# Optimization experiments

Measured on AMD Instinct MI355X. Metric: run time of the kernel, lower is better.

The kernel has to match this reference:

```python
import jax, jax.numpy as jnp
import numpy as np

B, S, D = 4, 1024, 2048
NH, NKV, HD = 16, 8, 128
N_EXP, TOP_K, RANK, ALPHA = 4, 2, 16, 32
LORA_SCALE = ALPHA / RANK
EPS = 1e-6
NEG_INF = -1e9


def setup_inputs() -> dict:
    key = jax.random.key(0)
    ks = jax.random.split(key, 12)
    inv_freq = 1.0 / (10000.0 ** (jnp.arange(0, HD, 2, dtype=jnp.float32) / HD))
    pos = jnp.arange(S, dtype=jnp.float32)
    freqs = pos[:, None] * inv_freq[None, :]            # [S, HD/2]
    emb = jnp.concatenate([freqs, freqs], axis=-1)      # [S, HD]
    cos = jnp.broadcast_to(jnp.cos(emb)[None], (B, S, HD))
    sin = jnp.broadcast_to(jnp.sin(emb)[None], (B, S, HD))
    s = 0.02
    return {
        "hidden_states": jax.random.normal(ks[0], (B, S, D), jnp.float32),
        "cos": cos,
        "sin": sin,
        "Wq": jax.random.normal(ks[1], (NH * HD, D), jnp.float32) * s,
        "Wk": jax.random.normal(ks[2], (NKV * HD, D), jnp.float32) * s,
        "Wv": jax.random.normal(ks[3], (NKV * HD, D), jnp.float32) * s,
        "Wo": jax.random.normal(ks[4], (D, NH * HD), jnp.float32) * s,
        "q_norm_w": jnp.ones((HD,), jnp.float32),
        "k_norm_w": jnp.ones((HD,), jnp.float32),
        "gate_w": jax.random.normal(ks[5], (N_EXP, D), jnp.float32) * s,
        "loraA": jax.random.normal(ks[6], (N_EXP, RANK, NH * HD), jnp.float32) * s,
        "loraB": jax.random.normal(ks[7], (N_EXP, D, RANK), jnp.float32) * s,
    }


def _rms_norm(x, w):
    # per-head-dim RMSNorm (Qwen3 style), computed in fp32
    var = jnp.mean(jnp.square(x.astype(jnp.float32)), axis=-1, keepdims=True)
    return (x.astype(jnp.float32) * jax.lax.rsqrt(var + EPS)).astype(x.dtype) * w


def _rotate_half(x):
    x1, x2 = jnp.split(x, 2, axis=-1)
    return jnp.concatenate([-x2, x1], axis=-1)


def reference(hidden_states, cos, sin, Wq, Wk, Wv, Wo, q_norm_w, k_norm_w, gate_w, loraA, loraB):
    b, s, d = hidden_states.shape
    scaling = HD ** -0.5

    # ---- router (top-k of softmax over 4 experts) ----
    flat = hidden_states.reshape(-1, d)                       # [T, D]
    router_logits = flat @ gate_w.T                           # [T, E]
    probs = jax.nn.softmax(router_logits.astype(jnp.float32), axis=-1)
    top_w, top_idx = jax.lax.top_k(probs, TOP_K)              # [T, K]
    top_w = top_w.astype(hidden_states.dtype)
    # dense per-expert weight: [T, E]
    expert_w = jnp.sum(jax.nn.one_hot(top_idx, N_EXP, dtype=top_w.dtype) * top_w[..., None], axis=1)

    # ---- QKV projections + per-head RMSNorm ----
    q = (hidden_states @ Wq.T).reshape(b, s, NH, HD)
    k = (hidden_states @ Wk.T).reshape(b, s, NKV, HD)
    v = (hidden_states @ Wv.T).reshape(b, s, NKV, HD)
    q = _rms_norm(q, q_norm_w).transpose(0, 2, 1, 3)          # [B, NH, S, HD]
    k = _rms_norm(k, k_norm_w).transpose(0, 2, 1, 3)          # [B, NKV, S, HD]
    v = v.transpose(0, 2, 1, 3)

    # ---- RoPE ----
    c, sn = cos[:, None], sin[:, None]                        # [B, 1, S, HD]
    q = q * c + _rotate_half(q) * sn
    k = k * c + _rotate_half(k) * sn

    # ---- GQA repeat + eager attention ----
    n_rep = NH // NKV
    k = jnp.repeat(k, n_rep, axis=1)
    v = jnp.repeat(v, n_rep, axis=1)
    attn = jnp.einsum('bhqd,bhkd->bhqk', q, k) * scaling
    causal = jnp.tril(jnp.ones((s, s), bool))
    attn = jnp.where(causal[None, None], attn, NEG_INF)
    attn_w = jax.nn.softmax(attn.astype(jnp.float32), axis=-1).astype(q.dtype)
    attn_out = jnp.einsum('bhqk,bhkd->bqhd', attn_w, v).reshape(b, s, NH * HD)

    # ---- base output projection + LoRA expert mixture ----
    base = attn_out @ Wo.T                                    # [B, S, D]
    x = attn_out.reshape(-1, NH * HD)                         # [T, NH*HD]
    h = jnp.einsum('td,erd->ter', x, loraA)                   # [T, E, R]
    delta = jnp.einsum('ter,edr->ted', h, loraB) * LORA_SCALE # [T, E, D]
    expert_out = jnp.einsum('te,ted->td', expert_w, delta).reshape(b, s, d)

    return base + expert_out
```

## Files before the change

kernel.cpp:

```cpp
#include <hip/hip_runtime.h>
#include <hip/hip_bf16.h>

#define S_LEN   1024
#define BATCH   4
#define DMODEL  2048
#define NHEADS  16
#define NKVH    8
#define HEADD   128
#define NTOK    4096
#define QKV_CH  4096

typedef __bf16 bf16x8 __attribute__((ext_vector_type(8)));
typedef float  f32x4  __attribute__((ext_vector_type(4)));

__device__ __forceinline__ float bf2f(unsigned short u) {
    return __uint_as_float(((unsigned)u) << 16);
}
__device__ __forceinline__ ushort f2bu(float f) {
    union { __hip_bfloat16 h; ushort u; } c;
    c.h = __float2bfloat16(f);
    return c.u;
}
__device__ __forceinline__ void gl_lds16(const ushort* g, ushort* l) {
    __builtin_amdgcn_global_load_lds(
        (const __attribute__((address_space(1))) void*)g,
        (__attribute__((address_space(3))) void*)l,
        16, 0, 0);
}

__global__ __launch_bounds__(256) void wcast_kernel(const float* __restrict__ Wq,
                                                    const float* __restrict__ Wk,
                                                    const float* __restrict__ Wv,
                                                    const float* __restrict__ Wo,
                                                    const float* __restrict__ lA,
                                                    __hip_bfloat16* __restrict__ wqkv,
                                                    __hip_bfloat16* __restrict__ wo,
                                                    __hip_bfloat16* __restrict__ acat) {
    int i = blockIdx.x * 256 + threadIdx.x;
    const float* src; __hip_bfloat16* dst; int off;
    if (i < 1048576)      { src = Wq; dst = wqkv;           off = i; }
    else if (i < 1572864) { src = Wk; dst = wqkv + 4194304; off = i - 1048576; }
    else if (i < 2097152) { src = Wv; dst = wqkv + 6291456; off = i - 1572864; }
    else if (i < 3145728) { src = Wo; dst = wo;             off = i - 2097152; }
    else if (i < 3178496) { src = lA; dst = acat;           off = i - 3145728; }
    else return;
    float4 v = ((const float4*)src)[off];
    union { ushort4 u; __hip_bfloat16 h[4]; } r;
    r.h[0] = __float2bfloat16(v.x);
    r.h[1] = __float2bfloat16(v.y);
    r.h[2] = __float2bfloat16(v.z);
    r.h[3] = __float2bfloat16(v.w);
    ((ushort4*)dst)[off] = r.u;
}

__global__ __launch_bounds__(256) void btrans_kernel(const float* __restrict__ lB,
                                                     const float* __restrict__ cosb,
                                                     const float* __restrict__ sinb,
                                                     ushort* __restrict__ Bt,
                                                     float4* __restrict__ cs4) {
    if (blockIdx.x < 512) {
        int idx = blockIdx.x * 256 + threadIdx.x;
        int d = idx >> 6, er = idx & 63;
        int e = er >> 4, r = er & 15;
        Bt[idx] = f2bu(lB[((size_t)e * DMODEL + d) * 16 + r]);
    } else {
        int idx = (blockIdx.x - 512) * 256 + threadIdx.x;
        int s = idx >> 6, d0 = idx & 63;
        const float* cp = cosb + (size_t)s * HEADD;
        const float* sp = sinb + (size_t)s * HEADD;
        cs4[idx] = make_float4(cp[d0], cp[d0 + 64], sp[d0], sp[d0 + 64]);
    }
}

__global__ __launch_bounds__(256) void gatecast_kernel(const float* __restrict__ X,
                                                       const float* __restrict__ GW,
                                                       __hip_bfloat16* __restrict__ Xb,
                                                       float* __restrict__ EW) {
    __shared__ float red[4][257];
    const int t = blockIdx.x, tid = threadIdx.x;
    const float* x = X + (size_t)t * DMODEL;
    __hip_bfloat16* xb = Xb + (size_t)t * DMODEL;
    float p0 = 0.f, p1 = 0.f, p2 = 0.f, p3 = 0.f;
#pragma unroll
    for (int c = 0; c < 2; c++) {
        int i4 = tid + c * 256;
        float4 v = ((const float4*)x)[i4];
        union { ushort4 u; __hip_bfloat16 h[4]; } r;
        r.h[0] = __float2bfloat16(v.x);
        r.h[1] = __float2bfloat16(v.y);
        r.h[2] = __float2bfloat16(v.z);
        r.h[3] = __float2bfloat16(v.w);
        ((ushort4*)xb)[i4] = r.u;
        int d = i4 * 4;
        const float* g0 = GW + d;
        p0 += v.x * g0[0] + v.y * g0[1] + v.z * g0[2] + v.w * g0[3];
        const float* g1 = GW + DMODEL + d;
        p1 += v.x * g1[0] + v.y * g1[1] + v.z * g1[2] + v.w * g1[3];
        const float* g2 = GW + 2 * DMODEL + d;
        p2 += v.x * g2[0] + v.y * g2[1] + v.z * g2[2] + v.w * g2[3];
        const float* g3 = GW + 3 * DMODEL + d;
        p3 += v.x * g3[0] + v.y * g3[1] + v.z * g3[2] + v.w * g3[3];
    }
    red[0][tid] = p0; red[1][tid] = p1; red[2][tid] = p2; red[3][tid] = p3;
    __syncthreads();
    for (int s = 128; s > 0; s >>= 1) {
        if (tid < s) {
            red[0][tid] += red[0][tid + s];
            red[1][tid] += red[1][tid + s];
            red[2][tid] += red[2][tid + s];
            red[3][tid] += red[3][tid + s];
        }
        __syncthreads();
    }
    if (tid == 0) {
        float l[4] = { red[0][0], red[1][0], red[2][0], red[3][0] };
        float mx = fmaxf(fmaxf(l[0], l[1]), fmaxf(l[2], l[3]));
        float pe[4], sum = 0.f;
        for (int e = 0; e < 4; e++) { pe[e] = __expf(l[e] - mx); sum += pe[e]; }
        float inv = 1.0f / sum;
        for (int e = 0; e < 4; e++) pe[e] *= inv;
        int i1 = 0;
        for (int e = 1; e < 4; e++) if (pe[e] > pe[i1]) i1 = e;
        int i2 = -1;
        for (int e = 0; e < 4; e++) if (e != i1 && (i2 < 0 || pe[e] > pe[i2])) i2 = e;
        float o[4] = {0.f, 0.f, 0.f, 0.f};
        o[i1] = pe[i1]; o[i2] = pe[i2];
        float* ew = EW + (size_t)t * 4;
        ew[0] = o[0]; ew[1] = o[1]; ew[2] = o[2]; ew[3] = o[3];
    }
}

#define LDSA0 0
#define LDSB0 16384
#define LDSA1 32768
#define LDSB1 49152

#define FENCE_BAR() do { asm volatile("" ::: "memory"); __builtin_amdgcn_s_barrier(); } while (0)

__device__ __forceinline__ void stage_half(const ushort* src, ushort* dst, size_t ld) {
    gl_lds16(src, dst);
    gl_lds16(src + (size_t)64 * ld, dst + 4096);
}

#define PHASE_MFMA_PRE()  do { \
    asm volatile("" ::: "memory"); \
    __builtin_amdgcn_s_barrier(); \
    asm volatile("s_waitcnt lgkmcnt(0)" ::: "memory"); \
    __builtin_amdgcn_sched_barrier(0); \
    __builtin_amdgcn_s_setprio(1); } while (0)

#define PHASE_MFMA_POST() do { \
    __builtin_amdgcn_s_setprio(0); } while (0)

__device__ __forceinline__ void ktile(const ushort* As, const ushort* Bs,
                                      f32x4 (&acc)[8][4],
                                      int aBase, int bBase, int cs0, int cs1,
                                      const ushort* s1s, ushort* s1d, bool s12en,
                                      const ushort* s2s, ushort* s2d,
                                      const ushort* s3s, ushort* s3d, bool s34en,
                                      const ushort* s4s, ushort* s4d,
                                      int K, bool lastVm)
{
    bf16x8 a0[4][2], a1[4][2], b0[2][2], b1[2][2];

#pragma unroll
    for (int ii = 0; ii < 4; ii++) {
        a0[ii][0] = *(const bf16x8*)(As + aBase + ii * 2048 + cs0);
        a0[ii][1] = *(const bf16x8*)(As + aBase + ii * 2048 + cs1);
    }
#pragma unroll
    for (int jj = 0; jj < 2; jj++) {
        b0[jj][0] = *(const bf16x8*)(Bs + bBase + jj * 4096 + cs0);
        b0[jj][1] = *(const bf16x8*)(Bs + bBase + jj * 4096 + cs1);
    }
    if (s12en) stage_half(s1s, s1d, K);
    asm volatile("s_waitcnt lgkmcnt(8)" ::: "memory");
    PHASE_MFMA_PRE();
#pragma unroll
    for (int k = 0; k < 2; k++)
#pragma unroll
        for (int ii = 0; ii < 4; ii++)
#pragma unroll
            for (int jj = 0; jj < 2; jj++)
                acc[ii][2 * jj] = __builtin_amdgcn_mfma_f32_16x16x32_bf16(
                    a0[ii][k], b0[jj][k], acc[ii][2 * jj], 0, 0, 0);
    PHASE_MFMA_POST();
    FENCE_BAR();

#pragma unroll
    for (int jj = 0; jj < 2; jj++) {
        b1[jj][0] = *(const bf16x8*)(Bs + bBase + 8192 + jj * 4096 + cs0);
        b1[jj][1] = *(const bf16x8*)(Bs + bBase + 8192 + jj * 4096 + cs1);
    }
    if (s12en) stage_half(s2s, s2d, K);
    PHASE_MFMA_PRE();
#pragma unroll
    for (int k = 0; k < 2; k++)
#pragma unroll
        for (int ii = 0; ii < 4; ii++)
#pragma unroll
            for (int jj = 0; jj < 2; jj++)
                acc[ii][1 + 2 * jj] = __builtin_amdgcn_mfma_f32_16x16x32_bf16(
                    a0[ii][k], b1[jj][k], acc[ii][1 + 2 * jj], 0, 0, 0);
    PHASE_MFMA_POST();
    FENCE_BAR();

#pragma unroll
    for (int ii = 0; ii < 4; ii++) {
        a1[ii][0] = *(const bf16x8*)(As + aBase + 8192 + ii * 2048 + cs0);
        a1[ii][1] = *(const bf16x8*)(As + aBase + 8192 + ii * 2048 + cs1);
    }
    if (s34en) stage_half(s3s, s3d, K);
    PHASE_MFMA_PRE();
#pragma unroll
    for (int k = 0; k < 2; k++)
#pragma unroll
        for (int ii = 0; ii < 4; ii++)
#pragma unroll
            for (int jj = 0; jj < 2; jj++)
                acc[4 + ii][2 * jj] = __builtin_amdgcn_mfma_f32_16x16x32_bf16(
                    a1[ii][k], b0[jj][k], acc[4 + ii][2 * jj], 0, 0, 0);
    PHASE_MFMA_POST();
    FENCE_BAR();

    if (s34en) stage_half(s4s, s4d, K);
    asm volatile("" ::: "memory");
    __builtin_amdgcn_s_barrier();
    __builtin_amdgcn_sched_barrier(0);
    __builtin_amdgcn_s_setprio(1);
#pragma unroll
    for (int k = 0; k < 2; k++)
#pragma unroll
        for (int ii = 0; ii < 4; ii++)
#pragma unroll
            for (int jj = 0; jj < 2; jj++)
                acc[4 + ii][1 + 2 * jj] = __builtin_amdgcn_mfma_f32_16x16x32_bf16(
                    a1[ii][k], b1[jj][k], acc[4 + ii][1 + 2 * jj], 0, 0, 0);
    __builtin_amdgcn_s_setprio(0);
    if (lastVm) { asm volatile("s_waitcnt vmcnt(0)" ::: "memory"); }
    else        { asm volatile("s_waitcnt vmcnt(4)" ::: "memory"); }
    __builtin_amdgcn_s_barrier();
}

__global__ __launch_bounds__(512, 2) void gemm256(const ushort* __restrict__ A,
                                                  const ushort* __restrict__ B,
                                                  const float4* __restrict__ cs4,
                                                  const float* __restrict__ qnw,
                                                  const float* __restrict__ knw,
                                                  ushort* __restrict__ Qb,
                                                  ushort* __restrict__ Kb,
                                                  ushort* __restrict__ Vt,
                                                  int K) {
    __shared__ __align__(16) ushort lds[65536];
    const int tid  = threadIdx.x;
    const int wave = tid >> 6, lane = tid & 63;
    const int l16  = lane & 15, quad = lane >> 4;
    const int wm = wave >> 2, wn = wave & 3;

    const int wg0 = blockIdx.x;
    const int swz = (wg0 & 7) * 32 + (wg0 >> 3);
    const int m0 = (swz >> 4) * 256, n0 = (swz & 15) * 256;

    const int srow = tid >> 3;
    const int scol = ((tid & 7) * 8) ^ ((srow & 7) << 3);
    const ushort* aSrc = A + (size_t)(m0 + srow) * K + scol;
    const ushort* bSrc = B + (size_t)(n0 + srow) * K + scol;

    const int aBase = (wm * 16 + l16) * 64;
    const int bBase = (wn * 16 + l16) * 64;
    const int cs0 = ((0 + quad) ^ (l16 & 7)) * 8;
    const int cs1 = ((4 + quad) ^ (l16 & 7)) * 8;

    f32x4 acc[8][4];
#pragma unroll
    for (int i = 0; i < 8; i++)
#pragma unroll
        for (int j = 0; j < 4; j++) acc[i][j] = (f32x4){0.f, 0.f, 0.f, 0.f};

    const int NT = K >> 6;

    const ushort* A0s = lds + LDSA0;
    const ushort* B0s = lds + LDSB0;
    const ushort* A1s = lds + LDSA1;
    const ushort* B1s = lds + LDSB1;

    stage_half(aSrc,                     lds + LDSA0 + tid * 8, K);
    stage_half(aSrc + (size_t)128 * K,   lds + LDSA0 + 8192 + tid * 8, K);
    stage_half(bSrc,                     lds + LDSB0 + tid * 8, K);
    stage_half(bSrc + (size_t)128 * K,   lds + LDSB0 + 8192 + tid * 8, K);
    stage_half(aSrc + 64,                lds + LDSA1 + tid * 8, K);
    stage_half(bSrc + 64,                lds + LDSB1 + tid * 8, K);
    asm volatile("s_waitcnt vmcnt(4)" ::: "memory");
    __builtin_amdgcn_s_barrier();

    for (int t = 0; t + 1 < NT; t += 2) {
        const bool s34 = (t + 2) < NT, s78 = (t + 3) < NT;
        const int k1 = (t + 1) * 64, k2 = (t + 2) * 64, k3 = (t + 3) * 64;

        ktile(A0s, B0s, acc, aBase, bBase, cs0, cs1,
              aSrc + (size_t)128 * K + k1, lds + LDSA1 + 8192 + tid * 8, true,
              bSrc + (size_t)128 * K + k1, lds + LDSB1 + 8192 + tid * 8,
              aSrc + k2,                   lds + LDSA0 + tid * 8, s34,
              bSrc + k2,                   lds + LDSB0 + tid * 8,
              K, !s34);

        ktile(A1s, B1s, acc, aBase, bBase, cs0, cs1,
              aSrc + (size_t)128 * K + k2, lds + LDSA0 + 8192 + tid * 8, s34,
              bSrc + (size_t)128 * K + k2, lds + LDSB0 + 8192 + tid * 8,
              aSrc + k3,                   lds + LDSA1 + tid * 8, s78,
              bSrc + k3,                   lds + LDSB1 + tid * 8,
              K, !s78);
    }

    const int nb = n0 >> 8;
    if (nb < 12) {
        const bool isQ = (nb < 8);
        const float scale = isQ ? 0.08838834764831845f : 1.0f;
        const float* nw = isQ ? qnw : knw;
        const int d0 = wn * 16 + l16;
        const float w0 = nw[d0] * scale, w1 = nw[d0 + 64] * scale;
        const int h0 = isQ ? (n0 >> 7) : ((n0 - 2048) >> 7);
        const int nh = isQ ? 16 : 8;
        ushort* gbase = isQ ? Qb : Kb;
        float* fsq = (float*)(lds + 32768);
        const float4* cvrow = cs4 + ((m0 & 1023) * 64 + d0);

#pragma unroll
        for (int half = 0; half < 2; half++) {
#pragma unroll
            for (int i2 = 0; i2 < 4; i2++)
#pragma unroll
                for (int r = 0; r < 4; r++) {
                    const int i = half * 4 + i2;
                    const int r128 = i2 * 32 + wm * 16 + quad * 4 + r;
#pragma unroll
                    for (int h = 0; h < 2; h++) {
                        float x1 = acc[i][h][r], x2 = acc[i][h + 2][r];
                        float p = x1 * x1 + x2 * x2;
                        p += __shfl_xor(p, 1);
                        p += __shfl_xor(p, 2);
                        p += __shfl_xor(p, 4);
                        p += __shfl_xor(p, 8);
                        if (l16 == 0) fsq[(r128 * 2 + h) * 4 + wn] = p;
                    }
                }
            __syncthreads();

#pragma unroll
            for (int i2 = 0; i2 < 4; i2++)
#pragma unroll
                for (int r = 0; r < 4; r++) {
                    const int i = half * 4 + i2;
                    const int r128 = i2 * 32 + wm * 16 + quad * 4 + r;
                    const float4 cv = cvrow[(size_t)(half * 128 + r128) * 64];
                    const int sw = ((r128 >> 2) & 3) << 4;
                    ushort* lrow = lds + r128 * 256;
#pragma unroll
                    for (int h = 0; h < 2; h++) {
                        const float* q4 = fsq + (r128 * 2 + h) * 4;
                        float ssq = q4[0] + q4[1] + q4[2] + q4[3];
                        float rstd = rsqrtf(ssq * (1.0f / 128.0f) + 1e-6f);
                        float n1 = acc[i][h][r] * rstd * w0;
                        float n2 = acc[i][h + 2][r] * rstd * w1;
                        lrow[(h * 128 + d0) ^ sw]      = f2bu(n1 * cv.x - n2 * cv.z);
                        lrow[(h * 128 + d0 + 64) ^ sw] = f2bu(n2 * cv.y + n1 * cv.w);
                    }
                }
            __syncthreads();

#pragma unroll
            for (int g = 0; g < 8; g++) {
                int gg = tid + g * 512;
                int row = gg >> 5, colg = gg & 31;
                int col8 = colg * 8;
                int sw = ((row >> 2) & 3) << 4;
                uint4 v = *(const uint4*)(lds + row * 256 + (col8 ^ sw));
                int head = col8 >> 7, d = col8 & 127;
                int tok = m0 + half * 128 + row;
                int b = tok >> 10, s = tok & 1023;
                *(uint4*)(gbase + ((size_t)((b * nh + h0 + head) * 1024 + s)) * HEADD + d) = v;
            }
            __syncthreads();
        }
    } else {
#pragma unroll
        for (int i = 0; i < 8; i++)
#pragma unroll
            for (int j = 0; j < 4; j++) {
                int coll = (j & 1) * 128 + (j >> 1) * 64 + wn * 16 + l16;
                int xr = (coll & 7) << 3;
#pragma unroll
                for (int r = 0; r < 4; r++) {
                    int rowl = (i & 3) * 32 + (i >> 2) * 128 + wm * 16 + quad * 4 + r;
                    lds[coll * 256 + (rowl ^ xr)] = f2bu(acc[i][j][r]);
                }
            }
        __syncthreads();
        const int b = m0 >> 10, s0 = m0 & 1023;
        const int kv0 = (n0 - 3072) >> 7;
#pragma unroll
        for (int g = 0; g < 16; g++) {
            int gg = tid + g * 512;
            int d = gg >> 5, sg = gg & 31;
            uint4 v = *(const uint4*)(lds + d * 256 + ((sg * 8) ^ ((d & 7) << 3)));
            int kv = kv0 + (d >> 7), dh = d & 127;
            *(uint4*)(Vt + ((size_t)((b * 8 + kv) * 128 + dh)) * 1024 + s0 + sg * 8) = v;
        }
    }
}

#define WO_A0 0
#define WO_A1 16384
#define WO_B0 32768
#define WO_B1 40960

__device__ __forceinline__ void wo_tile(const ushort* As, const ushort* Bs,
                                        f32x4 (&acc)[8][2],
                                        int aBase, int bBase, int cs0, int cs1,
                                        const ushort* s1s, ushort* s1d, size_t s1ld, bool s1en,
                                        const ushort* s2as, ushort* s2ad,
                                        const ushort* s2bs, ushort* s2bd, size_t s2ld, bool s2en,
                                        bool lastVm)
{
    bf16x8 a0[4][2], a1[4][2], b[2][2];

#pragma unroll
    for (int ii = 0; ii < 4; ii++) {
        a0[ii][0] = *(const bf16x8*)(As + aBase + ii * 2048 + cs0);
        a0[ii][1] = *(const bf16x8*)(As + aBase + ii * 2048 + cs1);
    }
#pragma unroll
    for (int jj = 0; jj < 2; jj++) {
        b[jj][0] = *(const bf16x8*)(Bs + bBase + jj * 4096 + cs0);
        b[jj][1] = *(const bf16x8*)(Bs + bBase + jj * 4096 + cs1);
    }
    if (s1en) stage_half(s1s, s1d, s1ld);
    asm volatile("s_waitcnt lgkmcnt(8)" ::: "memory");
    PHASE_MFMA_PRE();
#pragma unroll
    for (int k = 0; k < 2; k++)
#pragma unroll
        for (int ii = 0; ii < 4; ii++)
#pragma unroll
            for (int jj = 0; jj < 2; jj++)
                acc[ii][jj] = __builtin_amdgcn_mfma_f32_16x16x32_bf16(
                    a0[ii][k], b[jj][k], acc[ii][jj], 0, 0, 0);
    PHASE_MFMA_POST();
    FENCE_BAR();

#pragma unroll
    for (int ii = 0; ii < 4; ii++) {
        a1[ii][0] = *(const bf16x8*)(As + aBase + 8192 + ii * 2048 + cs0);
        a1[ii][1] = *(const bf16x8*)(As + aBase + 8192 + ii * 2048 + cs1);
    }
    if (s2en) { stage_half(s2as, s2ad, s2ld); stage_half(s2bs, s2bd, s2ld); }
    PHASE_MFMA_PRE();
#pragma unroll
    for (int k = 0; k < 2; k++)
#pragma unroll
        for (int ii = 0; ii < 4; ii++)
#pragma unroll
            for (int jj = 0; jj < 2; jj++)
                acc[4 + ii][jj] = __builtin_amdgcn_mfma_f32_16x16x32_bf16(
                    a1[ii][k], b[jj][k], acc[4 + ii][jj], 0, 0, 0);
    PHASE_MFMA_POST();
    if (lastVm) { asm volatile("s_waitcnt vmcnt(0)" ::: "memory"); }
    else        { asm volatile("s_waitcnt vmcnt(4)" ::: "memory"); }
    __builtin_amdgcn_s_barrier();
}

__global__ __launch_bounds__(512, 2) void gemm_wo(const ushort* __restrict__ A,
                                                  const ushort* __restrict__ B,
                                                  const ushort* __restrict__ A2,
                                                  const ushort* __restrict__ B2,
                                                  float* __restrict__ C) {
    __shared__ __align__(16) ushort lds[49152];
    const int tid  = threadIdx.x;
    const int wave = tid >> 6, lane = tid & 63;
    const int l16  = lane & 15, quad = lane >> 4;
    const int wm = wave >> 2, wn = wave & 3;
    const int K = DMODEL, N = DMODEL;

    const int wg0 = blockIdx.x;
    const int swz = (wg0 & 7) * 32 + (wg0 >> 3);
    const int m0 = (swz >> 4) * 256, n0 = (swz & 15) * 128;

    const int srow = tid >> 3;
    const int scol = ((tid & 7) * 8) ^ ((srow & 7) << 3);
    const ushort* aSrc  = A  + (size_t)(m0 + srow) * K + scol;
    const ushort* bSrc  = B  + (size_t)(n0 + srow) * K + scol;
    const ushort* a2Src = A2 + (size_t)(m0 + srow) * 64 + scol;
    const ushort* b2Src = B2 + (size_t)(n0 + srow) * 64 + scol;

    const int aBase = (wm * 16 + l16) * 64;
    const int bBase = (wn * 16 + l16) * 64;
    const int cs0 = ((0 + quad) ^ (l16 & 7)) * 8;
    const int cs1 = ((4 + quad) ^ (l16 & 7)) * 8;

    f32x4 acc[8][2];
#pragma unroll
    for (int i = 0; i < 8; i++)
#pragma unroll
        for (int j = 0; j < 2; j++) acc[i][j] = (f32x4){0.f, 0.f, 0.f, 0.f};

    const ushort* A0s = lds + WO_A0;
    const ushort* B0s = lds + WO_B0;
    const ushort* A1s = lds + WO_A1;
    const ushort* B1s = lds + WO_B1;

    stage_half(aSrc,                   lds + WO_A0 + tid * 8, K);
    stage_half(aSrc + (size_t)128 * K, lds + WO_A0 + 8192 + tid * 8, K);
    stage_half(bSrc,                   lds + WO_B0 + tid * 8, K);
    stage_half(aSrc + 64,              lds + WO_A1 + tid * 8, K);
    stage_half(bSrc + 64,              lds + WO_B1 + tid * 8, K);
    asm volatile("s_waitcnt vmcnt(4)" ::: "memory");
    __builtin_amdgcn_s_barrier();

    for (int t = 0; t < 32; t += 2) {
        const int u1 = t + 1, u2 = t + 2, u3 = t + 3;
        const bool l2 = (u2 == 32);
        const bool s3en = (u3 <= 32);

        const ushort* s2as = l2 ? a2Src : (aSrc + (size_t)u2 * 64);
        const ushort* s2bs = l2 ? b2Src : (bSrc + (size_t)u2 * 64);
        const size_t  s2ld = l2 ? (size_t)64 : (size_t)K;
        wo_tile(A0s, B0s, acc, aBase, bBase, cs0, cs1,
                aSrc + (size_t)128 * K + (size_t)u1 * 64, lds + WO_A1 + 8192 + tid * 8, K, true,
                s2as, lds + WO_A0 + tid * 8,
                s2bs, lds + WO_B0 + tid * 8, s2ld, true,
                false);

        const ushort* s1s = l2 ? (a2Src + (size_t)128 * 64)
                               : (aSrc + (size_t)128 * K + (size_t)u2 * 64);
        const size_t  s1ld = l2 ? (size_t)64 : (size_t)K;
        wo_tile(A1s, B1s, acc, aBase, bBase, cs0, cs1,
                s1s, lds + WO_A0 + 8192 + tid * 8, s1ld, true,
                aSrc + (size_t)u3 * 64, lds + WO_A1 + tid * 8,
                bSrc + (size_t)u3 * 64, lds + WO_B1 + tid * 8, K, s3en,
                !s3en);
    }
    wo_tile(A0s, B0s, acc, aBase, bBase, cs0, cs1,
            nullptr, nullptr, K, false,
            nullptr, nullptr, nullptr, nullptr, K, false,
            true);

    float* crow = C + (size_t)(m0 + wm * 16 + quad * 4) * N + n0 + wn * 16 + l16;
#pragma unroll
    for (int i = 0; i < 8; i++) {
        float* cpi = crow + (size_t)((i & 3) * 32 + (i >> 2) * 128) * N;
#pragma unroll
        for (int r = 0; r < 4; r++)
#pragma unroll
            for (int jj = 0; jj < 2; jj++)
                cpi[(size_t)r * N + jj * 64] = acc[i][jj][r];
    }
}

__global__ __launch_bounds__(256) void lora_h_kernel(const ushort* __restrict__ X,
                                                     const ushort* __restrict__ Acat,
                                                     const float* __restrict__ EW,
                                                     ushort* __restrict__ G) {
    __shared__ ushort As[64 * 64];
    __shared__ ushort Bs[64 * 64];
    const int tid = threadIdx.x;
    const int wave = tid >> 6, lane = tid & 63;
    const int l16 = lane & 15, quad = lane >> 4;
    const int m0 = blockIdx.x * 64;

    f32x4 acc[4];
#pragma unroll
    for (int nt = 0; nt < 4; nt++) acc[nt] = (f32x4){0.f, 0.f, 0.f, 0.f};

    const int r1 = tid >> 3;
    const int scol = ((tid & 7) * 8) ^ ((r1 & 7) << 3);
    const int cs0 = ((0 + quad) ^ (l16 & 7)) * 8;
    const int cs1 = ((4 + quad) ^ (l16 & 7)) * 8;

    for (int k0 = 0; k0 < DMODEL; k0 += 64) {
        __syncthreads();
        gl_lds16(X + (size_t)(m0 + r1) * DMODEL + k0 + scol, As + tid * 8);
        gl_lds16(X + (size_t)(m0 + 32 + r1) * DMODEL + k0 + scol, As + 2048 + tid * 8);
        gl_lds16(Acat + (size_t)r1 * DMODEL + k0 + scol, Bs + tid * 8);
        gl_lds16(Acat + (size_t)(32 + r1) * DMODEL + k0 + scol, Bs + 2048 + tid * 8);
        __syncthreads();
        bf16x8 af0 = *(const bf16x8*)(As + (wave * 16 + l16) * 64 + cs0);
        bf16x8 af1 = *(const bf16x8*)(As + (wave * 16 + l16) * 64 + cs1);
#pragma unroll
        for (int nt = 0; nt < 4; nt++) {
            bf16x8 b0 = *(const bf16x8*)(Bs + (nt * 16 + l16) * 64 + cs0);
            acc[nt] = __builtin_amdgcn_mfma_f32_16x16x32_bf16(af0, b0, acc[nt], 0, 0, 0);
            bf16x8 b1 = *(const bf16x8*)(Bs + (nt * 16 + l16) * 64 + cs1);
            acc[nt] = __builtin_amdgcn_mfma_f32_16x16x32_bf16(af1, b1, acc[nt], 0, 0, 0);
        }
    }
#pragma unroll
    for (int nt = 0; nt < 4; nt++)
#pragma unroll
        for (int r = 0; r < 4; r++) {
            int m = m0 + wave * 16 + quad * 4 + r;
            float wsc = 2.0f * EW[(size_t)m * 4 + nt];
            G[(size_t)m * 64 + nt * 16 + l16] = f2bu(acc[nt][r] * wsc);
        }
}

#define VPITCH 72
__global__ __launch_bounds__(256) void fattn_kernel(const ushort* __restrict__ Qb,
                                                    const ushort* __restrict__ Kb,
                                                    const ushort* __restrict__ Vt,
                                                    __hip_bfloat16* __restrict__ O) {
    __shared__ __align__(16) ushort Ks[64 * 128];
    __shared__ __align__(16) ushort Vs[128 * 64];
    __shared__ __align__(16) ushort Ps[4 * 16 * VPITCH];
    const int tid = threadIdx.x;
    const int wq = tid >> 6, lane = tid & 63;
    const int l16 = lane & 15, quad = lane >> 4;
    const int qblk = 15 - (blockIdx.x >> 6);
    const int bh = blockIdx.x & 63;
    const int b = bh >> 4, h = bh & 15;
    const int kvb = b * 8 + (h >> 1);
    const int q0 = qblk * 64;
    const int qbase = q0 + wq * 16;

    bf16x8 qf[4];
    const ushort* qrow = Qb + ((size_t)bh * S_LEN + qbase + l16) * HEADD;
#pragma unroll
    for (int kt = 0; kt < 4; kt++)
        qf[kt] = *(const bf16x8*)(qrow + kt * 32 + quad * 8);

    f32x4 oacc[8];
#pragma unroll
    for (int dt = 0; dt < 8; dt++) oacc[dt] = (f32x4){0.f, 0.f, 0.f, 0.f};
    float l[4] = { 0.f, 0.f, 0.f, 0.f };

    const ushort* kbase = Kb + (size_t)kvb * S_LEN * HEADD;
    const ushort* vbase = Vt + (size_t)kvb * HEADD * S_LEN;
    const int ntiles = qblk + 1;

    const int kr = tid >> 4, kc = ((tid & 15) * 8) ^ ((( tid >> 4) & 7) << 3);
    const int vr = tid >> 3, vc = ((tid & 7) * 8) ^ ((( tid >> 3) & 7) << 3);
    const int xrK = (l16 & 7) << 3;

    for (int kb = 0; kb < ntiles; kb++) {
        const int k0 = kb * 64;
        __syncthreads();
#pragma unroll
        for (int c = 0; c < 4; c++) {
            gl_lds16(kbase + (size_t)(k0 + c * 16 + kr) * HEADD + kc, Ks + c * 2048 + tid * 8);
            gl_lds16(vbase + (size_t)(c * 32 + vr) * S_LEN + k0 + vc, Vs + c * 2048 + tid * 8);
        }
        asm volatile("s_waitcnt vmcnt(0)" ::: "memory");
        __builtin_amdgcn_s_barrier();

        f32x4 sacc[4];
#pragma unroll
        for (int nt = 0; nt < 4; nt++) sacc[nt] = (f32x4){0.f, 0.f, 0.f, 0.f};
        __builtin_amdgcn_s_setprio(1);
#pragma unroll
        for (int kt = 0; kt < 4; kt++) {
#pragma unroll
            for (int nt = 0; nt < 4; nt++) {
                bf16x8 kf = *(const bf16x8*)(Ks + (nt * 16 + l16) * 128 + ((kt * 32 + quad * 8) ^ xrK));
                sacc[nt] = __builtin_amdgcn_mfma_f32_16x16x32_bf16(qf[kt], kf, sacc[nt], 0, 0, 0);
            }
        }
        __builtin_amdgcn_s_setprio(0);

#pragma unroll
        for (int r = 0; r < 4; r++) {
            const int qg = qbase + quad * 4 + r;
#pragma unroll
            for (int nt = 0; nt < 4; nt++) {
                int kg = k0 + nt * 16 + l16;
                float p = (kg <= qg) ? __expf(sacc[nt][r]) : 0.f;
                l[r] += p;
                Ps[wq * 16 * VPITCH + (quad * 4 + r) * VPITCH + nt * 16 + l16] = f2bu(p);
            }
        }

        __builtin_amdgcn_s_setprio(1);
#pragma unroll
        for (int kt2 = 0; kt2 < 2; kt2++) {
            bf16x8 pf = *(const bf16x8*)(Ps + wq * 16 * VPITCH + l16 * VPITCH + kt2 * 32 + quad * 8);
#pragma unroll
            for (int dt = 0; dt < 8; dt++) {
                bf16x8 vf = *(const bf16x8*)(Vs + (dt * 16 + l16) * 64 + ((kt2 * 32 + quad * 8) ^ xrK));
                oacc[dt] = __builtin_amdgcn_mfma_f32_16x16x32_bf16(pf, vf, oacc[dt], 0, 0, 0);
            }
        }
        __builtin_amdgcn_s_setprio(0);
    }

#pragma unroll
    for (int r = 0; r < 4; r++) {
        float lr = l[r];
        lr += __shfl_xor(lr, 1);
        lr += __shfl_xor(lr, 2);
        lr += __shfl_xor(lr, 4);
        lr += __shfl_xor(lr, 8);
        float inv = 1.0f / lr;
        size_t base = ((size_t)(b * S_LEN + qbase + quad * 4 + r)) * (NHEADS * HEADD) + h * HEADD;
#pragma unroll
        for (int dt = 0; dt < 8; dt++)
            O[base + dt * 16 + l16] = __float2bfloat16(oacc[dt][r] * inv);
    }
}

extern "C" void kernel_launch(void* const* d_in, const int* in_sizes, int n_in,
                              void* d_out, int out_size, void* d_ws, size_t ws_size,
                              hipStream_t stream) {
    const float* hidden = (const float*)d_in[0];
    const float* cosb   = (const float*)d_in[1];
    const float* sinb   = (const float*)d_in[2];
    const float* Wq     = (const float*)d_in[3];
    const float* Wk     = (const float*)d_in[4];
    const float* Wv     = (const float*)d_in[5];
    const float* Wo     = (const float*)d_in[6];
    const float* qnw    = (const float*)d_in[7];
    const float* knw    = (const float*)d_in[8];
    const float* gw     = (const float*)d_in[9];
    const float* lA     = (const float*)d_in[10];
    const float* lB     = (const float*)d_in[11];
    float* out = (float*)d_out;

    char* ws = (char*)d_ws;
    __hip_bfloat16* hid_bf  = (__hip_bfloat16*)ws;
    __hip_bfloat16* wqkv_bf = (__hip_bfloat16*)(ws + (16u << 20));
    __hip_bfloat16* wo_bf   = (__hip_bfloat16*)(ws + (32u << 20));
    ushort*         Qb      = (ushort*)(ws + (40u << 20));
    ushort*         Kb      = (ushort*)(ws + (56u << 20));
    ushort*         Vt      = (ushort*)(ws + (64u << 20));
    __hip_bfloat16* attn_bf = (__hip_bfloat16*)(ws + (72u << 20));
    ushort*         Acat    = (ushort*)(ws + (104u << 20));
    ushort*         Bt      = (ushort*)(ws + (104u << 20) + (256u << 10));
    ushort*         G       = (ushort*)(ws + (104u << 20) + (512u << 10));
    float*          ew      = (float*)(ws + (105u << 20));
    float4*         cs4     = (float4*)(ws + (106u << 20));

    wcast_kernel<<<12416, 256, 0, stream>>>(Wq, Wk, Wv, Wo, lA,
                                            wqkv_bf, wo_bf, (__hip_bfloat16*)Acat);
    gatecast_kernel<<<4096, 256, 0, stream>>>(hidden, gw, hid_bf, ew);
    btrans_kernel<<<768, 256, 0, stream>>>(lB, cosb, sinb, Bt, cs4);

    gemm256<<<256, 512, 0, stream>>>((const ushort*)hid_bf, (const ushort*)wqkv_bf,
                                     cs4, qnw, knw, Qb, Kb, Vt, DMODEL);

    fattn_kernel<<<1024, 256, 0, stream>>>(Qb, Kb, Vt, attn_bf);

    lora_h_kernel<<<64, 256, 0, stream>>>((const ushort*)attn_bf, Acat, ew, G);

    gemm_wo<<<256, 512, 0, stream>>>((const ushort*)attn_bf, (const ushort*)wo_bf,
                                     G, Bt, out);
}
```

Measured before the change: 316.0 us.

## Merge prep kernels into one launch and double-buffer K/V tiles in attention

Folds the three preprocessing kernels (weight cast, hidden cast plus router, LoRA-B transpose plus cos/sin packing) into a single kernel with block-range dispatch, removing two launch gaps. The flash-attention kernel now double-buffers K and V tiles in LDS and prefetches the next tile with global_load_lds while computing on the current one, waiting only for the older batch of loads. This doubles K/V LDS use, which may lower occupancy, and adds a barrier at the end of each iteration. The merged kernel's early return in the cast branch sits alongside __syncthreads in another branch, but that is uniform per block so it stays safe.

```diff
diff --git a/kernel.cpp b/kernel.cpp
--- a/kernel.cpp
+++ b/kernel.cpp
@@ -28,105 +28,108 @@
         16, 0, 0);
 }
 
-__global__ __launch_bounds__(256) void wcast_kernel(const float* __restrict__ Wq,
-                                                    const float* __restrict__ Wk,
-                                                    const float* __restrict__ Wv,
-                                                    const float* __restrict__ Wo,
-                                                    const float* __restrict__ lA,
-                                                    __hip_bfloat16* __restrict__ wqkv,
-                                                    __hip_bfloat16* __restrict__ wo,
-                                                    __hip_bfloat16* __restrict__ acat) {
-    int i = blockIdx.x * 256 + threadIdx.x;
-    const float* src; __hip_bfloat16* dst; int off;
-    if (i < 1048576)      { src = Wq; dst = wqkv;           off = i; }
-    else if (i < 1572864) { src = Wk; dst = wqkv + 4194304; off = i - 1048576; }
-    else if (i < 2097152) { src = Wv; dst = wqkv + 6291456; off = i - 1572864; }
-    else if (i < 3145728) { src = Wo; dst = wo;             off = i - 2097152; }
-    else if (i < 3178496) { src = lA; dst = acat;           off = i - 3145728; }
-    else return;
-    float4 v = ((const float4*)src)[off];
-    union { ushort4 u; __hip_bfloat16 h[4]; } r;
-    r.h[0] = __float2bfloat16(v.x);
-    r.h[1] = __float2bfloat16(v.y);
-    r.h[2] = __float2bfloat16(v.z);
-    r.h[3] = __float2bfloat16(v.w);
-    ((ushort4*)dst)[off] = r.u;
-}
-
-__global__ __launch_bounds__(256) void btrans_kernel(const float* __restrict__ lB,
-                                                     const float* __restrict__ cosb,
-                                                     const float* __restrict__ sinb,
-                                                     ushort* __restrict__ Bt,
-                                                     float4* __restrict__ cs4) {
-    if (blockIdx.x < 512) {
-        int idx = blockIdx.x * 256 + threadIdx.x;
-        int d = idx >> 6, er = idx & 63;
-        int e = er >> 4, r = er & 15;
-        Bt[idx] = f2bu(lB[((size_t)e * DMODEL + d) * 16 + r]);
-    } else {
-        int idx = (blockIdx.x - 512) * 256 + threadIdx.x;
-        int s = idx >> 6, d0 = idx & 63;
-        const float* cp = cosb + (size_t)s * HEADD;
-        const float* sp = sinb + (size_t)s * HEADD;
-        cs4[idx] = make_float4(cp[d0], cp[d0 + 64], sp[d0], sp[d0 + 64]);
-    }
-}
-
-__global__ __launch_bounds__(256) void gatecast_kernel(const float* __restrict__ X,
-                                                       const float* __restrict__ GW,
-                                                       __hip_bfloat16* __restrict__ Xb,
-                                                       float* __restrict__ EW) {
+__global__ __launch_bounds__(256) void prep_kernel(const float* __restrict__ Wq,
+                                                   const float* __restrict__ Wk,
+                                                   const float* __restrict__ Wv,
+                                                   const float* __restrict__ Wo,
+                                                   const float* __restrict__ lA,
+                                                   const float* __restrict__ lB,
+                                                   const float* __restrict__ cosb,
+                                                   const float* __restrict__ sinb,
+                                                   const float* __restrict__ X,
+                                                   const float* __restrict__ GW,
+                                                   __hip_bfloat16* __restrict__ wqkv,
+                                                   __hip_bfloat16* __restrict__ wo,
+                                                   __hip_bfloat16* __restrict__ acat,
+                                                   __hip_bfloat16* __restrict__ Xb,
+                                                   float* __restrict__ EW,
+                                                   ushort* __restrict__ Bt,
+                                                   float4* __restrict__ cs4) {
     __shared__ float red[4][257];
-    const int t = blockIdx.x, tid = threadIdx.x;
-    const float* x = X + (size_t)t * DMODEL;
-    __hip_bfloat16* xb = Xb + (size_t)t * DMODEL;
-    float p0 = 0.f, p1 = 0.f, p2 = 0.f, p3 = 0.f;
-#pragma unroll
-    for (int c = 0; c < 2; c++) {
-        int i4 = tid + c * 256;
-        float4 v = ((const float4*)x)[i4];
+    const int blk = blockIdx.x, tid = threadIdx.x;
+
+    if (blk < 12416) {
+        int i = blk * 256 + tid;
+        const float* src; __hip_bfloat16* dst; int off;
+        if (i < 1048576)      { src = Wq; dst = wqkv;           off = i; }
+        else if (i < 1572864) { src = Wk; dst = wqkv + 4194304; off = i - 1048576; }
+        else if (i < 2097152) { src = Wv; dst = wqkv + 6291456; off = i - 1572864; }
+        else if (i < 3145728) { src = Wo; dst = wo;             off = i - 2097152; }
+        else if (i < 3178496) { src = lA; dst = acat;           off = i - 3145728; }
+        else return;
+        float4 v = ((const float4*)src)[off];
         union { ushort4 u; __hip_bfloat16 h[4]; } r;
         r.h[0] = __float2bfloat16(v.x);
         r.h[1] = __float2bfloat16(v.y);
         r.h[2] = __float2bfloat16(v.z);
         r.h[3] = __float2bfloat16(v.w);
-        ((ushort4*)xb)[i4] = r.u;
-        int d = i4 * 4;
-        const float* g0 = GW + d;
-        p0 += v.x * g0[0] + v.y * g0[1] + v.z * g0[2] + v.w * g0[3];
-        const float* g1 = GW + DMODEL + d;
-        p1 += v.x * g1[0] + v.y * g1[1] + v.z * g1[2] + v.w * g1[3];
-        const float* g2 = GW + 2 * DMODEL + d;
-        p2 += v.x * g2[0] + v.y * g2[1] + v.z * g2[2] + v.w * g2[3];
-        const float* g3 = GW + 3 * DMODEL + d;
-        p3 += v.x * g3[0] + v.y * g3[1] + v.z * g3[2] + v.w * g3[3];
-    }
-    red[0][tid] = p0; red[1][tid] = p1; red[2][tid] = p2; red[3][tid] = p3;
-    __syncthreads();
-    for (int s = 128; s > 0; s >>= 1) {
-        if (tid < s) {
-            red[0][tid] += red[0][tid + s];
-            red[1][tid] += red[1][tid + s];
-            red[2][tid] += red[2][tid + s];
-            red[3][tid] += red[3][tid + s];
-        }
+        ((ushort4*)dst)[off] = r.u;
+    } else if (blk < 16512) {
+        const int t = blk - 12416;
+        const float* x = X + (size_t)t * DMODEL;
+        __hip_bfloat16* xb = Xb + (size_t)t * DMODEL;
+        float p0 = 0.f, p1 = 0.f, p2 = 0.f, p3 = 0.f;
+#pragma unroll
+        for (int c = 0; c < 2; c++) {
+            int i4 = tid + c * 256;
+            float4 v = ((const float4*)x)[i4];
+            union { ushort4 u; __hip_bfloat16 h[4]; } r;
+            r.h[0] = __float2bfloat16(v.x);
+            r.h[1] = __float2bfloat16(v.y);
+            r.h[2] = __float2bfloat16(v.z);
+            r.h[3] = __float2bfloat16(v.w);
+            ((ushort4*)xb)[i4] = r.u;
+            int d = i4 * 4;
+            const float* g0 = GW + d;
+            p0 += v.x * g0[0] + v.y * g0[1] + v.z * g0[2] + v.w * g0[3];
+            const float* g1 = GW + DMODEL + d;
+            p1 += v.x * g1[0] + v.y * g1[1] + v.z * g1[2] + v.w * g1[3];
+            const float* g2 = GW + 2 * DMODEL + d;
+            p2 += v.x * g2[0] + v.y * g2[1] + v.z * g2[2] + v.w * g2[3];
+            const float* g3 = GW + 3 * DMODEL + d;
+            p3 += v.x * g3[0] + v.y * g3[1] + v.z * g3[2] + v.w * g3[3];
+        }
+        red[0][tid] = p0; red[1][tid] = p1; red[2][tid] = p2; red[3][tid] = p3;
         __syncthreads();
-    }
-    if (tid == 0) {
-        float l[4] = { red[0][0], red[1][0], red[2][0], red[3][0] };
-        float mx = fmaxf(fmaxf(l[0], l[1]), fmaxf(l[2], l[3]));
-        float pe[4], sum = 0.f;
-        for (int e = 0; e < 4; e++) { pe[e] = __expf(l[e] - mx); sum += pe[e]; }
-        float inv = 1.0f / sum;
-        for (int e = 0; e < 4; e++) pe[e] *= inv;
-        int i1 = 0;
-        for (int e = 1; e < 4; e++) if (pe[e] > pe[i1]) i1 = e;
-        int i2 = -1;
-        for (int e = 0; e < 4; e++) if (e != i1 && (i2 < 0 || pe[e] > pe[i2])) i2 = e;
-        float o[4] = {0.f, 0.f, 0.f, 0.f};
-        o[i1] = pe[i1]; o[i2] = pe[i2];
-        float* ew = EW + (size_t)t * 4;
-        ew[0] = o[0]; ew[1] = o[1]; ew[2] = o[2]; ew[3] = o[3];
+        for (int s = 128; s > 0; s >>= 1) {
+            if (tid < s) {
+                red[0][tid] += red[0][tid + s];
+                red[1][tid] += red[1][tid + s];
+                red[2][tid] += red[2][tid + s];
+                red[3][tid] += red[3][tid + s];
+            }
+            __syncthreads();
+        }
+        if (tid == 0) {
+            float l[4] = { red[0][0], red[1][0], red[2][0], red[3][0] };
+            float mx = fmaxf(fmaxf(l[0], l[1]), fmaxf(l[2], l[3]));
+            float pe[4], sum = 0.f;
+            for (int e = 0; e < 4; e++) { pe[e] = __expf(l[e] - mx); sum += pe[e]; }
+            float inv = 1.0f / sum;
+            for (int e = 0; e < 4; e++) pe[e] *= inv;
+            int i1 = 0;
+            for (int e = 1; e < 4; e++) if (pe[e] > pe[i1]) i1 = e;
+            int i2 = -1;
+            for (int e = 0; e < 4; e++) if (e != i1 && (i2 < 0 || pe[e] > pe[i2])) i2 = e;
+            float o[4] = {0.f, 0.f, 0.f, 0.f};
+            o[i1] = pe[i1]; o[i2] = pe[i2];
+            float* ew = EW + (size_t)t * 4;
+            ew[0] = o[0]; ew[1] = o[1]; ew[2] = o[2]; ew[3] = o[3];
+        }
+    } else {
+        const int bblk = blk - 16512;
+        if (bblk < 512) {
+            int idx = bblk * 256 + tid;
+            int d = idx >> 6, er = idx & 63;
+            int e = er >> 4, r = er & 15;
+            Bt[idx] = f2bu(lB[((size_t)e * DMODEL + d) * 16 + r]);
+        } else {
+            int idx = (bblk - 512) * 256 + tid;
+            int s = idx >> 6, d0 = idx & 63;
+            const float* cp = cosb + (size_t)s * HEADD;
+            const float* sp = sinb + (size_t)s * HEADD;
+            cs4[idx] = make_float4(cp[d0], cp[d0 + 64], sp[d0], sp[d0 + 64]);
+        }
     }
 }
 
@@ -608,8 +611,8 @@
                                                     const ushort* __restrict__ Kb,
                                                     const ushort* __restrict__ Vt,
                                                     __hip_bfloat16* __restrict__ O) {
-    __shared__ __align__(16) ushort Ks[64 * 128];
-    __shared__ __align__(16) ushort Vs[128 * 64];
+    __shared__ __align__(16) ushort Ks[2][64 * 128];
+    __shared__ __align__(16) ushort Vs[2][128 * 64];
     __shared__ __align__(16) ushort Ps[4 * 16 * VPITCH];
     const int tid = threadIdx.x;
     const int wq = tid >> 6, lane = tid & 63;
@@ -640,16 +643,31 @@
     const int vr = tid >> 3, vc = ((tid & 7) * 8) ^ ((( tid >> 3) & 7) << 3);
     const int xrK = (l16 & 7) << 3;
 
+#pragma unroll
+    for (int c = 0; c < 4; c++) {
+        gl_lds16(kbase + (size_t)(c * 16 + kr) * HEADD + kc, &Ks[0][c * 2048 + tid * 8]);
+        gl_lds16(vbase + (size_t)(c * 32 + vr) * S_LEN + vc, &Vs[0][c * 2048 + tid * 8]);
+    }
+
     for (int kb = 0; kb < ntiles; kb++) {
+        const int cur = kb & 1;
         const int k0 = kb * 64;
-        __syncthreads();
-#pragma unroll
-        for (int c = 0; c < 4; c++) {
-            gl_lds16(kbase + (size_t)(k0 + c * 16 + kr) * HEADD + kc, Ks + c * 2048 + tid * 8);
-            gl_lds16(vbase + (size_t)(c * 32 + vr) * S_LEN + k0 + vc, Vs + c * 2048 + tid * 8);
-        }
-        asm volatile("s_waitcnt vmcnt(0)" ::: "memory");
+        if (kb + 1 < ntiles) {
+            const int k0n = k0 + 64;
+#pragma unroll
+            for (int c = 0; c < 4; c++) {
+                gl_lds16(kbase + (size_t)(k0n + c * 16 + kr) * HEADD + kc,
+                         &Ks[cur ^ 1][c * 2048 + tid * 8]);
+                gl_lds16(vbase + (size_t)(c * 32 + vr) * S_LEN + k0n + vc,
+                         &Vs[cur ^ 1][c * 2048 + tid * 8]);
+            }
+            asm volatile("s_waitcnt vmcnt(8)" ::: "memory");
+        } else {
+            asm volatile("s_waitcnt vmcnt(0)" ::: "memory");
+        }
         __builtin_amdgcn_s_barrier();
+        const ushort* Kc = Ks[cur];
+        const ushort* Vc = Vs[cur];
 
         f32x4 sacc[4];
 #pragma unroll
@@ -659,7 +677,7 @@
         for (int kt = 0; kt < 4; kt++) {
 #pragma unroll
             for (int nt = 0; nt < 4; nt++) {
-                bf16x8 kf = *(const bf16x8*)(Ks + (nt * 16 + l16) * 128 + ((kt * 32 + quad * 8) ^ xrK));
+                bf16x8 kf = *(const bf16x8*)(Kc + (nt * 16 + l16) * 128 + ((kt * 32 + quad * 8) ^ xrK));
                 sacc[nt] = __builtin_amdgcn_mfma_f32_16x16x32_bf16(qf[kt], kf, sacc[nt], 0, 0, 0);
             }
         }
@@ -683,11 +701,13 @@
             bf16x8 pf = *(const bf16x8*)(Ps + wq * 16 * VPITCH + l16 * VPITCH + kt2 * 32 + quad * 8);
 #pragma unroll
             for (int dt = 0; dt < 8; dt++) {
-                bf16x8 vf = *(const bf16x8*)(Vs + (dt * 16 + l16) * 64 + ((kt2 * 32 + quad * 8) ^ xrK));
+                bf16x8 vf = *(const bf16x8*)(Vc + (dt * 16 + l16) * 64 + ((kt2 * 32 + quad * 8) ^ xrK));
                 oacc[dt] = __builtin_amdgcn_mfma_f32_16x16x32_bf16(pf, vf, oacc[dt], 0, 0, 0);
             }
         }
         __builtin_amdgcn_s_setprio(0);
+        asm volatile("" ::: "memory");
+        __builtin_amdgcn_s_barrier();
     }
 
 #pragma unroll
@@ -736,10 +756,10 @@
     float*          ew      = (float*)(ws + (105u << 20));
     float4*         cs4     = (float4*)(ws + (106u << 20));
 
-    wcast_kernel<<<12416, 256, 0, stream>>>(Wq, Wk, Wv, Wo, lA,
-                                            wqkv_bf, wo_bf, (__hip_bfloat16*)Acat);
-    gatecast_kernel<<<4096, 256, 0, stream>>>(hidden, gw, hid_bf, ew);
-    btrans_kernel<<<768, 256, 0, stream>>>(lB, cosb, sinb, Bt, cs4);
+    prep_kernel<<<17280, 256, 0, stream>>>(Wq, Wk, Wv, Wo, lA, lB, cosb, sinb,
+                                           hidden, gw,
+                                           wqkv_bf, wo_bf, (__hip_bfloat16*)Acat,
+                                           hid_bf, ew, Bt, cs4);
 
     gemm256<<<256, 512, 0, stream>>>((const ushort*)hid_bf, (const ushort*)wqkv_bf,
                                      cs4, qnw, knw, Qb, Kb, Vt, DMODEL);
```

Measured after the change: 313.3 us. No clear change (-0.8%).
